# Performance work log

Hardware: AMD Instinct MI355X
Metric: run time of the kernel (lower is better)

## Reference

```python
import jax, jax.numpy as jnp
import numpy as np


def setup_inputs() -> dict:
    key = jax.random.key(0)
    k1, k2, k3 = jax.random.split(key, 3)
    p = 4096
    target = jax.random.normal(k1, (p, p), dtype=jnp.float32)
    source = jax.random.normal(k2, (p, p), dtype=jnp.float32)
    W_beta = jax.random.uniform(k3, (p, p), dtype=jnp.float32)
    return {"target": target, "source": source, "W_beta": W_beta}


def reference(target, source, W_beta):
    # X = target, Y = source (module-level names in the original).
    # denominator inner loop: sum_i X[i] . X[i] == ||X||_F^2 (scalar),
    # recomputed p^2 times in the original; computed once here.
    s = jnp.sum(target * target)
    W = W_beta.sum(axis=1)                       # [p]
    W2 = W * W                                   # [p]
    scale = W2 / (s * W2 + 1.0)                  # [p]
    G = jnp.matmul(source, target.T)             # [p,p], G[i,j] = Y[i] . X[j]
    W_matrix = scale[:, None] * G                # [p,p]
    primary = jnp.matmul(W_matrix, target) - source
    loss = jnp.sqrt(jnp.sum(jnp.square(jnp.matmul(W_beta, primary))))
    return loss, W_matrix
```

## Files before the change

kernel.cpp:

```cpp
#include <hip/hip_runtime.h>
#include <hip/hip_bf16.h>

#define PDIM 4096
#define PPN ((size_t)PDIM * (size_t)PDIM)

typedef __attribute__((ext_vector_type(8))) short bf16x8;
typedef __attribute__((ext_vector_type(4))) float floatx4;
typedef __attribute__((ext_vector_type(8))) int int8v;

__device__ __forceinline__ void load_lds16(const void* g, void* l) {
  __builtin_amdgcn_global_load_lds(
      (const __attribute__((address_space(1))) void*)g,
      (__attribute__((address_space(3))) void*)l, 16, 0, 0);
}

__device__ __forceinline__ unsigned short bf16bits(float f) {
  __hip_bfloat16 h = __float2bfloat16(f);
  return *(unsigned short*)&h;
}

__device__ __forceinline__ unsigned char fp8byte(float v) {
  return (unsigned char)(__builtin_amdgcn_cvt_pk_fp8_f32(v, v, 0, false) & 0xff);
}
__device__ __forceinline__ unsigned int fp8x4(float a, float b, float c, float d) {
  int v = __builtin_amdgcn_cvt_pk_fp8_f32(a, b, 0, false);
  v = __builtin_amdgcn_cvt_pk_fp8_f32(c, d, v, true);
  return (unsigned int)v;
}

__global__ void sumsq(const float4* __restrict__ x, float* __restrict__ acc) {
  float s = 0.f;
  const size_t n4 = PPN / 4;
  for (size_t i = (size_t)blockIdx.x * 256 + threadIdx.x; i < n4;
       i += (size_t)gridDim.x * 256) {
    const float4 v = x[i];
    s += v.x * v.x + v.y * v.y + v.z * v.z + v.w * v.w;
  }
#pragma unroll
  for (int off = 32; off > 0; off >>= 1) s += __shfl_down(s, off);
  __shared__ float ws[4];
  if ((threadIdx.x & 63) == 0) ws[threadIdx.x >> 6] = s;
  __syncthreads();
  if (threadIdx.x == 0) atomicAdd(acc, ws[0] + ws[1] + ws[2] + ws[3]);
}

__global__ void cast_x(const float* __restrict__ src,
                       __hip_bfloat16* __restrict__ dstN,
                       unsigned char* __restrict__ dstT8) {
  __shared__ float tile[64][65];
  const int bx = blockIdx.x * 64, by = blockIdx.y * 64;
  const int tx = threadIdx.x & 15, ty = threadIdx.x >> 4;
#pragma unroll
  for (int r = 0; r < 4; ++r) {
    const int row = ty + r * 16;
    const float4 v = *(const float4*)&src[(size_t)(by + row) * PDIM + bx + tx * 4];
    tile[row][tx * 4 + 0] = v.x;
    tile[row][tx * 4 + 1] = v.y;
    tile[row][tx * 4 + 2] = v.z;
    tile[row][tx * 4 + 3] = v.w;
    ushort4 o;
    o.x = bf16bits(v.x); o.y = bf16bits(v.y); o.z = bf16bits(v.z); o.w = bf16bits(v.w);
    *(ushort4*)&dstN[(size_t)(by + row) * PDIM + bx + tx * 4] = o;
  }
  __syncthreads();
#pragma unroll
  for (int r = 0; r < 4; ++r) {
    const int i = ty + r * 16;
    *(unsigned int*)&dstT8[(size_t)(bx + i) * PDIM + by + tx * 4] =
        fp8x4(tile[tx * 4 + 0][i], tile[tx * 4 + 1][i],
              tile[tx * 4 + 2][i], tile[tx * 4 + 3][i]);
  }
}

__global__ void cast_y(const float* __restrict__ src,
                       __hip_bfloat16* __restrict__ dstN,
                       __hip_bfloat16* __restrict__ dstT) {
  __shared__ float tile[64][65];
  const int bx = blockIdx.x * 64, by = blockIdx.y * 64;
  const int tx = threadIdx.x & 15, ty = threadIdx.x >> 4;
#pragma unroll
  for (int r = 0; r < 4; ++r) {
    const int row = ty + r * 16;
    const float4 v = *(const float4*)&src[(size_t)(by + row) * PDIM + bx + tx * 4];
    tile[row][tx * 4 + 0] = v.x;
    tile[row][tx * 4 + 1] = v.y;
    tile[row][tx * 4 + 2] = v.z;
    tile[row][tx * 4 + 3] = v.w;
    ushort4 o;
    o.x = bf16bits(v.x); o.y = bf16bits(v.y); o.z = bf16bits(v.z); o.w = bf16bits(v.w);
    *(ushort4*)&dstN[(size_t)(by + row) * PDIM + bx + tx * 4] = o;
  }
  __syncthreads();
#pragma unroll
  for (int r = 0; r < 4; ++r) {
    const int i = ty + r * 16;
    ushort4 o;
    o.x = bf16bits(tile[tx * 4 + 0][i]);
    o.y = bf16bits(tile[tx * 4 + 1][i]);
    o.z = bf16bits(tile[tx * 4 + 2][i]);
    o.w = bf16bits(tile[tx * 4 + 3][i]);
    *(ushort4*)&dstT[(size_t)(bx + i) * PDIM + by + tx * 4] = o;
  }
}

__global__ void cast_wb_rows(const float* __restrict__ Wb,
                             unsigned char* __restrict__ Wb8,
                             const float* __restrict__ sAcc,
                             float* __restrict__ scale) {
  const size_t row = blockIdx.x;
  const float4* src = (const float4*)(Wb + row * PDIM);
  unsigned int* dst = (unsigned int*)(Wb8 + row * PDIM);
  float sum = 0.f;
#pragma unroll
  for (int it = 0; it < 4; ++it) {
    const int j = threadIdx.x + it * 256;
    const float4 v = src[j];
    sum += (v.x + v.y) + (v.z + v.w);
    dst[j] = fp8x4(v.x, v.y, v.z, v.w);
  }
#pragma unroll
  for (int off = 32; off > 0; off >>= 1) sum += __shfl_down(sum, off);
  __shared__ float ws[4];
  if ((threadIdx.x & 63) == 0) ws[threadIdx.x >> 6] = sum;
  __syncthreads();
  if (threadIdx.x == 0) {
    const float W = ws[0] + ws[1] + ws[2] + ws[3];
    const float w2 = W * W;
    scale[row] = w2 / ((*sAcc) * w2 + 1.0f);
  }
}

__device__ __forceinline__ void mfma_quad(floatx4 (&acc)[8][4], int mo, int no,
                                          const bf16x8 (&af)[8],
                                          const bf16x8 (&bf)[4]) {
  __builtin_amdgcn_s_setprio(1);
#pragma unroll
  for (int mi = 0; mi < 4; ++mi)
#pragma unroll
    for (int ni = 0; ni < 2; ++ni)
#pragma unroll
      for (int kk = 0; kk < 2; ++kk)
        acc[mo + mi][no + ni] = __builtin_amdgcn_mfma_f32_16x16x32_bf16(
            af[mi * 2 + kk], bf[ni * 2 + kk], acc[mo + mi][no + ni], 0, 0, 0);
  __builtin_amdgcn_s_setprio(0);
}

__device__ __forceinline__ void read_a(bf16x8 (&dst)[8], const char* base, int slot0) {
#pragma unroll
  for (int mi = 0; mi < 4; ++mi) {
    dst[mi * 2 + 0] = *(const bf16x8*)(base + mi * 2048 + slot0);
    dst[mi * 2 + 1] = *(const bf16x8*)(base + mi * 2048 + (slot0 ^ 64));
  }
}
__device__ __forceinline__ void read_b(bf16x8 (&dst)[4], const char* base, int slot0) {
#pragma unroll
  for (int ni = 0; ni < 2; ++ni) {
    dst[ni * 2 + 0] = *(const bf16x8*)(base + ni * 2048 + slot0);
    dst[ni * 2 + 1] = *(const bf16x8*)(base + ni * 2048 + (slot0 ^ 64));
  }
}

__global__ __launch_bounds__(512, 2)
void gemm_bf16_wm(const __hip_bfloat16* __restrict__ A,
                  const __hip_bfloat16* __restrict__ B,
                  const float* __restrict__ scale,
                  float* __restrict__ outF,
                  unsigned char* __restrict__ Wm8) {
  __shared__ __align__(16) char LDS[131072];

  const int tid = threadIdx.x;
  const int lane = tid & 63;
  const int wave = tid >> 6;
  const int wm = wave >> 2;
  const int wn = wave & 3;

  const int bid = blockIdx.x;
  const int swz = (bid & 7) * 32 + (bid >> 3);
  const int bx = swz & 15;
  const int by = swz >> 4;
  const size_t rowA0 = (size_t)by * 256;
  const size_t rowB0 = (size_t)bx * 256;

  const int srow = tid >> 3;
  const int scol = ((tid & 7) ^ (srow & 7)) << 4;
  const char* pA = (const char*)A + (rowA0 + srow) * 8192 + scol;
  const char* pB = (const char*)B + (rowB0 + srow) * 8192 + scol;
  const int ldsWav = wave * 1024;

  const int fr = lane & 15;
  const int kq = lane >> 4;
  const int slot0 = ((kq ^ (fr & 7)) << 4);
  const int aRowB = (wm * 64 + fr) * 128;
  const int bRowB = (wn * 32 + fr) * 128;

  floatx4 acc[8][4] = {};
  bf16x8 afLo[8], afHi[8], bLo[4], bHi[4];

  {
    char* dA0 = LDS + ldsWav;
    char* dB0 = LDS + 65536 + ldsWav;
    load_lds16(pA, dA0);                         load_lds16(pA + 524288, dA0 + 8192);
    load_lds16(pB, dB0);                         load_lds16(pB + 524288, dB0 + 8192);
    load_lds16(pB + 1048576, dB0 + 16384);       load_lds16(pB + 1572864, dB0 + 24576);
    load_lds16(pA + 1048576, dA0 + 16384);       load_lds16(pA + 1572864, dA0 + 24576);
    char* dA1 = dA0 + 32768;
    char* dB1 = dB0 + 32768;
    load_lds16(pA + 128, dA1);                   load_lds16(pA + 128 + 524288, dA1 + 8192);
    load_lds16(pB + 128, dB1);                   load_lds16(pB + 128 + 524288, dB1 + 8192);
    load_lds16(pB + 128 + 1048576, dB1 + 16384); load_lds16(pB + 128 + 1572864, dB1 + 24576);
    load_lds16(pA + 128 + 1048576, dA1 + 16384); load_lds16(pA + 128 + 1572864, dA1 + 24576);
  }
  asm volatile("s_waitcnt vmcnt(8)" ::: "memory");
  __builtin_amdgcn_s_barrier();
  read_a(afLo, (const char*)LDS + aRowB, slot0);
  read_b(bLo, (const char*)LDS + 65536 + bRowB, slot0);
  asm volatile("s_waitcnt lgkmcnt(0)" ::: "memory");
  __builtin_amdgcn_s_barrier();

  for (int t = 0; t < 64; ++t) {
    const int buf = (t & 1) << 15;
    const int tS = (t + 2) & 63;
    const char* sA = pA + (size_t)tS * 128;
    const char* sB = pB + (size_t)tS * 128;
    char* dA = LDS + buf + ldsWav;
    char* dB = LDS + 65536 + buf + ldsWav;
    const char* aRd  = LDS + buf + aRowB;
    const char* bRd  = LDS + 65536 + buf + bRowB;
    const char* aRdN = LDS + (buf ^ 32768) + aRowB;
    const char* bRdN = LDS + 65536 + (buf ^ 32768) + bRowB;

    load_lds16(sA, dA);
    load_lds16(sA + 524288, dA + 8192);
    mfma_quad(acc, 0, 0, afLo, bLo);
    read_b(bHi, bRd + 16384, slot0);
    __builtin_amdgcn_s_barrier();

    load_lds16(sB, dB);
    load_lds16(sB + 524288, dB + 8192);
    mfma_quad(acc, 0, 2, afLo, bHi);
    read_a(afHi, aRd + 16384, slot0);
    __builtin_amdgcn_s_barrier();

    asm volatile("s_waitcnt vmcnt(10)" ::: "memory");
    load_lds16(sB + 1048576, dB + 16384);
    load_lds16(sB + 1572864, dB + 24576);
    mfma_quad(acc, 4, 2, afHi, bHi);
    read_a(afLo, aRdN, slot0);
    __builtin_amdgcn_s_barrier();

    asm volatile("s_waitcnt vmcnt(6)" ::: "memory");
    load_lds16(sA + 1048576, dA + 16384);
    load_lds16(sA + 1572864, dA + 24576);
    mfma_quad(acc, 4, 0, afHi, bLo);
    read_b(bLo, bRdN, slot0);
    __builtin_amdgcn_s_barrier();
  }

  const int lr = (lane >> 4) << 2;
  const int lc = lane & 15;
#pragma unroll
  for (int mi = 0; mi < 8; ++mi) {
    const size_t rbase = rowA0 + (size_t)(mi >> 2) * 128 + wm * 64 + (mi & 3) * 16 + lr;
#pragma unroll
    for (int r = 0; r < 4; ++r) {
      const size_t row = rbase + r;
      const float sc = scale[row];
#pragma unroll
      for (int ni = 0; ni < 4; ++ni) {
        const size_t col = rowB0 + (size_t)(ni >> 1) * 128 + wn * 32 + (ni & 1) * 16 + lc;
        const float v = sc * acc[mi][ni][r];
        outF[row * PDIM + col] = v;
        Wm8[row * PDIM + col] = fp8byte(v * 131072.f);
      }
    }
  }
}

template <int MODE>
__global__ __launch_bounds__(256)
void gemm_fp8(const unsigned char* __restrict__ A,
              const unsigned char* __restrict__ B,
              const __hip_bfloat16* __restrict__ sub,
              unsigned char* __restrict__ outP,
              float* __restrict__ lossAcc) {
  __shared__ __align__(16) unsigned char As[128 * 128];
  __shared__ __align__(16) unsigned char Bs[128 * 128];

  const int tid = threadIdx.x;
  const int lane = tid & 63;
  const int wave = tid >> 6;
  const int wm = wave >> 1, wn = wave & 1;

  const size_t rowA0 = (size_t)blockIdx.y * 128;
  const size_t rowB0 = (size_t)blockIdx.x * 128;

  const unsigned char* gA[4];
  const unsigned char* gB[4];
  int ldsOff[4];
#pragma unroll
  for (int m = 0; m < 4; ++m) {
    const int ci = tid + m * 256;
    const int r = ci >> 3, s = ci & 7;
    const int cg = s ^ (r & 7);
    gA[m] = A + (rowA0 + (size_t)r) * PDIM + cg * 16;
    gB[m] = B + (rowB0 + (size_t)r) * PDIM + cg * 16;
    ldsOff[m] = m * 4096 + wave * 1024;
  }

  floatx4 acc[4][4] = {};

  const int fr = lane & 15;
  const int e = fr & 7;
  const int q2 = (lane >> 4) << 1;
  const int offLo = (q2 ^ e) << 4;
  const int offHi = ((q2 + 1) ^ e) << 4;
  const int abase = (wm * 64 + fr) * 128;
  const int bbase = (wn * 64 + fr) * 128;

  for (int kt = 0; kt < PDIM; kt += 128) {
#pragma unroll
    for (int m = 0; m < 4; ++m) load_lds16(gA[m] + kt, (char*)As + ldsOff[m]);
#pragma unroll
    for (int m = 0; m < 4; ++m) load_lds16(gB[m] + kt, (char*)Bs + ldsOff[m]);
    __syncthreads();

    union { int8v v; int4 h[2]; } af[4], bg[4];
#pragma unroll
    for (int mi = 0; mi < 4; ++mi) {
      af[mi].h[0] = *(const int4*)(As + abase + mi * 2048 + offLo);
      af[mi].h[1] = *(const int4*)(As + abase + mi * 2048 + offHi);
    }
#pragma unroll
    for (int ni = 0; ni < 4; ++ni) {
      bg[ni].h[0] = *(const int4*)(Bs + bbase + ni * 2048 + offLo);
      bg[ni].h[1] = *(const int4*)(Bs + bbase + ni * 2048 + offHi);
    }
#pragma unroll
    for (int mi = 0; mi < 4; ++mi)
#pragma unroll
      for (int ni = 0; ni < 4; ++ni)
        acc[mi][ni] = __builtin_amdgcn_mfma_scale_f32_16x16x128_f8f6f4(
            af[mi].v, bg[ni].v, acc[mi][ni],
            0 , 0 , 0, 0x7F7F7F7F, 0, 0x7F7F7F7F);
    __syncthreads();
  }

  const size_t row0 = rowA0 + wm * 64;
  const size_t col0 = rowB0 + wn * 64;
  const int lr = (lane >> 4) << 2;
  const int lc = lane & 15;

  if constexpr (MODE == 2) {
    float tot = 0.f;
#pragma unroll
    for (int mi = 0; mi < 4; ++mi)
#pragma unroll
      for (int ni = 0; ni < 4; ++ni)
#pragma unroll
        for (int r = 0; r < 4; ++r) tot += acc[mi][ni][r] * acc[mi][ni][r];
#pragma unroll
    for (int off = 32; off > 0; off >>= 1) tot += __shfl_down(tot, off);
    __shared__ float ws[4];
    if (lane == 0) ws[wave] = tot;
    __syncthreads();
    if (tid == 0) atomicAdd(lossAcc, ws[0] + ws[1] + ws[2] + ws[3]);
  } else {
    constexpr float INV = 1.f / 131072.f;
#pragma unroll
    for (int mi = 0; mi < 4; ++mi) {
#pragma unroll
      for (int r = 0; r < 4; ++r) {
        const size_t row = row0 + mi * 16 + lr + r;
#pragma unroll
        for (int ni = 0; ni < 4; ++ni) {
          const size_t col = col0 + ni * 16 + lc;
          const float v = acc[mi][ni][r] * INV - __bfloat162float(sub[row * PDIM + col]);
          outP[row * PDIM + col] = fp8byte(v);
        }
      }
    }
  }
}

__global__ void finalize(float* __restrict__ out, const float* __restrict__ acc) {
  if (threadIdx.x == 0) out[0] = sqrtf(*acc);
}

extern "C" void kernel_launch(void* const* d_in, const int* in_sizes, int n_in,
                              void* d_out, int out_size, void* d_ws, size_t ws_size,
                              hipStream_t stream) {
  const float* X  = (const float*)d_in[0];
  const float* Y  = (const float*)d_in[1];
  const float* Wb = (const float*)d_in[2];
  float* out = (float*)d_out;

  __hip_bfloat16* Xb   = (__hip_bfloat16*)d_ws;
  __hip_bfloat16* Yb   = Xb + PPN;
  __hip_bfloat16* YbT  = Yb + PPN;
  unsigned char*  XT8  = (unsigned char*)(YbT + PPN);
  unsigned char*  Wm8  = XT8 + PPN;
  unsigned char*  Wb8  = Wm8 + PPN;
  unsigned char*  PT8  = Wb8 + PPN;
  float* scale   = (float*)(PT8 + PPN);
  float* sAcc    = scale + PDIM;
  float* lossAcc = sAcc + 1;

  hipMemsetAsync(sAcc, 0, 2 * sizeof(float), stream);

  sumsq<<<1024, 256, 0, stream>>>((const float4*)X, sAcc);

  dim3 cgrid(PDIM / 64, PDIM / 64);
  cast_x<<<cgrid, 256, 0, stream>>>(X, Xb, XT8);
  cast_y<<<cgrid, 256, 0, stream>>>(Y, Yb, YbT);
  cast_wb_rows<<<PDIM, 256, 0, stream>>>(Wb, Wb8, sAcc, scale);

  gemm_bf16_wm<<<dim3(256), 512, 0, stream>>>(Yb, Xb, scale, out + 1, Wm8);

  dim3 ggrid(PDIM / 128, PDIM / 128);
  gemm_fp8<1><<<ggrid, 256, 0, stream>>>(XT8, Wm8, YbT, PT8, nullptr);
  gemm_fp8<2><<<ggrid, 256, 0, stream>>>(PT8, Wb8, nullptr, nullptr, lossAcc);

  finalize<<<1, 1, 0, stream>>>(out, lossAcc);
}
```

Baseline: 541.1 us.

## Restructure FP8 GEMMs into 256x256 tiles with double-buffered LDS pipeline

The two FP8 GEMM kernels move from 128x128 tiles with 4 waves and a single LDS buffer to 256x256 tiles with 8 waves, a 128 KB double-buffered LDS ring, and prefetch two k-steps ahead. MFMA quadrants are interleaved with LDS fragment reads and global-to-LDS loads, using explicit vmcnt waits and s_setprio. A block-index swizzle is added to improve L2 locality. The aim is to hide memory latency and raise data reuse per tile, at the cost of only 256 blocks, heavy LDS use, and fragile hand-tuned waitcnt ordering.

```diff
diff --git a/kernel.cpp b/kernel.cpp
--- a/kernel.cpp
+++ b/kernel.cpp
@@ -276,104 +276,167 @@
   }
 }
 
+union f8frag { int8v v; int4 h[2]; };
+
+__device__ __forceinline__ void mfma_quad8(floatx4 (&acc)[8][4], int mo, int no,
+                                           const f8frag (&af)[4],
+                                           const f8frag (&bf)[2]) {
+  __builtin_amdgcn_s_setprio(1);
+#pragma unroll
+  for (int mi = 0; mi < 4; ++mi)
+#pragma unroll
+    for (int ni = 0; ni < 2; ++ni)
+      acc[mo + mi][no + ni] = __builtin_amdgcn_mfma_scale_f32_16x16x128_f8f6f4(
+          af[mi].v, bf[ni].v, acc[mo + mi][no + ni],
+          0 , 0 , 0, 0x7F7F7F7F, 0, 0x7F7F7F7F);
+  __builtin_amdgcn_s_setprio(0);
+}
+
+__device__ __forceinline__ void read_a8(f8frag (&dst)[4], const char* base,
+                                        int offLo, int offHi) {
+#pragma unroll
+  for (int mi = 0; mi < 4; ++mi) {
+    dst[mi].h[0] = *(const int4*)(base + mi * 2048 + offLo);
+    dst[mi].h[1] = *(const int4*)(base + mi * 2048 + offHi);
+  }
+}
+__device__ __forceinline__ void read_b8(f8frag (&dst)[2], const char* base,
+                                        int offLo, int offHi) {
+#pragma unroll
+  for (int ni = 0; ni < 2; ++ni) {
+    dst[ni].h[0] = *(const int4*)(base + ni * 2048 + offLo);
+    dst[ni].h[1] = *(const int4*)(base + ni * 2048 + offHi);
+  }
+}
+
 template <int MODE>
-__global__ __launch_bounds__(256)
+__global__ __launch_bounds__(512, 2)
 void gemm_fp8(const unsigned char* __restrict__ A,
               const unsigned char* __restrict__ B,
               const __hip_bfloat16* __restrict__ sub,
               unsigned char* __restrict__ outP,
               float* __restrict__ lossAcc) {
-  __shared__ __align__(16) unsigned char As[128 * 128];
-  __shared__ __align__(16) unsigned char Bs[128 * 128];
+  __shared__ __align__(16) char LDS[131072];
 
   const int tid = threadIdx.x;
   const int lane = tid & 63;
   const int wave = tid >> 6;
-  const int wm = wave >> 1, wn = wave & 1;
-
-  const size_t rowA0 = (size_t)blockIdx.y * 128;
-  const size_t rowB0 = (size_t)blockIdx.x * 128;
-
-  const unsigned char* gA[4];
-  const unsigned char* gB[4];
-  int ldsOff[4];
-#pragma unroll
-  for (int m = 0; m < 4; ++m) {
-    const int ci = tid + m * 256;
-    const int r = ci >> 3, s = ci & 7;
-    const int cg = s ^ (r & 7);
-    gA[m] = A + (rowA0 + (size_t)r) * PDIM + cg * 16;
-    gB[m] = B + (rowB0 + (size_t)r) * PDIM + cg * 16;
-    ldsOff[m] = m * 4096 + wave * 1024;
-  }
-
-  floatx4 acc[4][4] = {};
+  const int wm = wave >> 2;
+  const int wn = wave & 3;
+
+  const int bid = blockIdx.x;
+  const int swz = (bid & 7) * 32 + (bid >> 3);
+  const int bx = swz & 15;
+  const int by = swz >> 4;
+  const size_t rowA0 = (size_t)by * 256;
+  const size_t rowB0 = (size_t)bx * 256;
+
+  const int srow = tid >> 3;
+  const int scol = ((tid & 7) ^ (srow & 7)) << 4;
+  const char* pA = (const char*)A + (rowA0 + srow) * 4096 + scol;
+  const char* pB = (const char*)B + (rowB0 + srow) * 4096 + scol;
+  const int ldsWav = wave * 1024;
 
   const int fr = lane & 15;
   const int e = fr & 7;
   const int q2 = (lane >> 4) << 1;
   const int offLo = (q2 ^ e) << 4;
   const int offHi = ((q2 + 1) ^ e) << 4;
-  const int abase = (wm * 64 + fr) * 128;
-  const int bbase = (wn * 64 + fr) * 128;
-
-  for (int kt = 0; kt < PDIM; kt += 128) {
-#pragma unroll
-    for (int m = 0; m < 4; ++m) load_lds16(gA[m] + kt, (char*)As + ldsOff[m]);
-#pragma unroll
-    for (int m = 0; m < 4; ++m) load_lds16(gB[m] + kt, (char*)Bs + ldsOff[m]);
-    __syncthreads();
-
-    union { int8v v; int4 h[2]; } af[4], bg[4];
-#pragma unroll
-    for (int mi = 0; mi < 4; ++mi) {
-      af[mi].h[0] = *(const int4*)(As + abase + mi * 2048 + offLo);
-      af[mi].h[1] = *(const int4*)(As + abase + mi * 2048 + offHi);
-    }
-#pragma unroll
-    for (int ni = 0; ni < 4; ++ni) {
-      bg[ni].h[0] = *(const int4*)(Bs + bbase + ni * 2048 + offLo);
-      bg[ni].h[1] = *(const int4*)(Bs + bbase + ni * 2048 + offHi);
-    }
-#pragma unroll
-    for (int mi = 0; mi < 4; ++mi)
-#pragma unroll
-      for (int ni = 0; ni < 4; ++ni)
-        acc[mi][ni] = __builtin_amdgcn_mfma_scale_f32_16x16x128_f8f6f4(
-            af[mi].v, bg[ni].v, acc[mi][ni],
-            0 , 0 , 0, 0x7F7F7F7F, 0, 0x7F7F7F7F);
-    __syncthreads();
-  }
-
-  const size_t row0 = rowA0 + wm * 64;
-  const size_t col0 = rowB0 + wn * 64;
+  const int aRowB = (wm * 64 + fr) * 128;
+  const int bRowB = (wn * 32 + fr) * 128;
+
+  floatx4 acc[8][4] = {};
+  f8frag afLo[4], afHi[4], bLo[2], bHi[2];
+
+  {
+    char* dA0 = LDS + ldsWav;
+    char* dB0 = LDS + 65536 + ldsWav;
+    load_lds16(pA, dA0);                        load_lds16(pA + 262144, dA0 + 8192);
+    load_lds16(pB, dB0);                        load_lds16(pB + 262144, dB0 + 8192);
+    load_lds16(pB + 524288, dB0 + 16384);       load_lds16(pB + 786432, dB0 + 24576);
+    load_lds16(pA + 524288, dA0 + 16384);       load_lds16(pA + 786432, dA0 + 24576);
+    char* dA1 = dA0 + 32768;
+    char* dB1 = dB0 + 32768;
+    load_lds16(pA + 128, dA1);                  load_lds16(pA + 128 + 262144, dA1 + 8192);
+    load_lds16(pB + 128, dB1);                  load_lds16(pB + 128 + 262144, dB1 + 8192);
+    load_lds16(pB + 128 + 524288, dB1 + 16384); load_lds16(pB + 128 + 786432, dB1 + 24576);
+    load_lds16(pA + 128 + 524288, dA1 + 16384); load_lds16(pA + 128 + 786432, dA1 + 24576);
+  }
+  asm volatile("s_waitcnt vmcnt(8)" ::: "memory");
+  __builtin_amdgcn_s_barrier();
+  read_a8(afLo, (const char*)LDS + aRowB, offLo, offHi);
+  read_b8(bLo, (const char*)LDS + 65536 + bRowB, offLo, offHi);
+  asm volatile("s_waitcnt lgkmcnt(0)" ::: "memory");
+  __builtin_amdgcn_s_barrier();
+
+  for (int t = 0; t < 32; ++t) {
+    const int buf = (t & 1) << 15;
+    const int tS = (t + 2) & 31;
+    const char* sA = pA + (size_t)tS * 128;
+    const char* sB = pB + (size_t)tS * 128;
+    char* dA = LDS + buf + ldsWav;
+    char* dB = LDS + 65536 + buf + ldsWav;
+    const char* aRd  = LDS + buf + aRowB;
+    const char* bRd  = LDS + 65536 + buf + bRowB;
+    const char* aRdN = LDS + (buf ^ 32768) + aRowB;
+    const char* bRdN = LDS + 65536 + (buf ^ 32768) + bRowB;
+
+    load_lds16(sA, dA);
+    load_lds16(sA + 262144, dA + 8192);
+    mfma_quad8(acc, 0, 0, afLo, bLo);
+    read_b8(bHi, bRd + 16384, offLo, offHi);
+    __builtin_amdgcn_s_barrier();
+
+    load_lds16(sB, dB);
+    load_lds16(sB + 262144, dB + 8192);
+    mfma_quad8(acc, 0, 2, afLo, bHi);
+    read_a8(afHi, aRd + 16384, offLo, offHi);
+    __builtin_amdgcn_s_barrier();
+
+    asm volatile("s_waitcnt vmcnt(10)" ::: "memory");
+    load_lds16(sB + 524288, dB + 16384);
+    load_lds16(sB + 786432, dB + 24576);
+    mfma_quad8(acc, 4, 2, afHi, bHi);
+    read_a8(afLo, aRdN, offLo, offHi);
+    __builtin_amdgcn_s_barrier();
+
+    asm volatile("s_waitcnt vmcnt(6)" ::: "memory");
+    load_lds16(sA + 524288, dA + 16384);
+    load_lds16(sA + 786432, dA + 24576);
+    mfma_quad8(acc, 4, 0, afHi, bLo);
+    read_b8(bLo, bRdN, offLo, offHi);
+    __builtin_amdgcn_s_barrier();
+  }
+
   const int lr = (lane >> 4) << 2;
   const int lc = lane & 15;
 
   if constexpr (MODE == 2) {
     float tot = 0.f;
 #pragma unroll
-    for (int mi = 0; mi < 4; ++mi)
+    for (int mi = 0; mi < 8; ++mi)
 #pragma unroll
       for (int ni = 0; ni < 4; ++ni)
 #pragma unroll
         for (int r = 0; r < 4; ++r) tot += acc[mi][ni][r] * acc[mi][ni][r];
 #pragma unroll
     for (int off = 32; off > 0; off >>= 1) tot += __shfl_down(tot, off);
-    __shared__ float ws[4];
+    __shared__ float ws[8];
     if (lane == 0) ws[wave] = tot;
     __syncthreads();
-    if (tid == 0) atomicAdd(lossAcc, ws[0] + ws[1] + ws[2] + ws[3]);
+    if (tid == 0)
+      atomicAdd(lossAcc, ws[0] + ws[1] + ws[2] + ws[3] + ws[4] + ws[5] + ws[6] + ws[7]);
   } else {
     constexpr float INV = 1.f / 131072.f;
 #pragma unroll
-    for (int mi = 0; mi < 4; ++mi) {
+    for (int mi = 0; mi < 8; ++mi) {
+      const size_t rbase = rowA0 + (size_t)(mi >> 2) * 128 + wm * 64 + (mi & 3) * 16 + lr;
 #pragma unroll
       for (int r = 0; r < 4; ++r) {
-        const size_t row = row0 + mi * 16 + lr + r;
+        const size_t row = rbase + r;
 #pragma unroll
         for (int ni = 0; ni < 4; ++ni) {
-          const size_t col = col0 + ni * 16 + lc;
+          const size_t col = rowB0 + (size_t)(ni >> 1) * 128 + wn * 32 + (ni & 1) * 16 + lc;
           const float v = acc[mi][ni][r] * INV - __bfloat162float(sub[row * PDIM + col]);
           outP[row * PDIM + col] = fp8byte(v);
         }
@@ -416,9 +479,8 @@
 
   gemm_bf16_wm<<<dim3(256), 512, 0, stream>>>(Yb, Xb, scale, out + 1, Wm8);
 
-  dim3 ggrid(PDIM / 128, PDIM / 128);
-  gemm_fp8<1><<<ggrid, 256, 0, stream>>>(XT8, Wm8, YbT, PT8, nullptr);
-  gemm_fp8<2><<<ggrid, 256, 0, stream>>>(PT8, Wb8, nullptr, nullptr, lossAcc);
+  gemm_fp8<1><<<dim3(256), 512, 0, stream>>>(XT8, Wm8, YbT, PT8, nullptr);
+  gemm_fp8<2><<<dim3(256), 512, 0, stream>>>(PT8, Wb8, nullptr, nullptr, lossAcc);
 
   finalize<<<1, 1, 0, stream>>>(out, lossAcc);
 }
```

New measurement: 520.6 us. -3.8%, faster.
